# Kernel optimization log

Measured on AMD Instinct MI355X. Metric: run time of the kernel, lower is better.

Reference implementation:

```python
import jax, jax.numpy as jnp
import numpy as np

B, C, T, H, W = 2, 256, 16, 32, 32
NH = 8
GROUPS = 32
EPS = 1e-6


def setup_inputs() -> dict:
    key = jax.random.key(0)
    ks = jax.random.split(key, 10)
    r = lambda k, shape: jax.random.normal(k, shape, dtype=jnp.float32) * 0.02
    return dict(
        x=jax.random.normal(ks[0], (B, C, T, H, W), dtype=jnp.float32),
        gn_gamma=jnp.ones((C,), jnp.float32),
        gn_beta=jnp.zeros((C,), jnp.float32),
        wq_s=r(ks[1], (C, C)), bq_s=jnp.zeros((C,), jnp.float32),
        wk_s=r(ks[2], (C, C)), bk_s=jnp.zeros((C,), jnp.float32),
        wv_s=r(ks[3], (C, C)), bv_s=jnp.zeros((C,), jnp.float32),
        wo_s=r(ks[4], (C, C)), bo_s=jnp.zeros((C,), jnp.float32),
        wq_t=r(ks[5], (C, C)),
        wk_t=r(ks[6], (C, C)),
        wv_t=r(ks[7], (C, C)),
        wf_t=r(ks[8], (C, C)), bf_t=jnp.zeros((C,), jnp.float32),
    )


def group_norm(x, gamma, beta):
    # x: (N, C, H, W), GroupNorm(32, eps=1e-6, affine)
    n, c, h, w = x.shape
    xg = x.reshape(n, GROUPS, c // GROUPS, h, w)
    mu = xg.mean(axis=(2, 3, 4), keepdims=True)
    var = xg.var(axis=(2, 3, 4), keepdims=True)
    xg = (xg - mu) * jax.lax.rsqrt(var + EPS)
    return xg.reshape(n, c, h, w) * gamma[None, :, None, None] + beta[None, :, None, None]


def spatial_attention(x, gn_gamma, gn_beta, wq, bq, wk, bk, wv, bv, wo, bo):
    # ldm SpatialSelfAttention: norm -> 1x1 conv q/k/v -> full HW self-attn -> 1x1 proj -> residual
    n, c, h, w = x.shape
    hf = group_norm(x, gn_gamma, gn_beta).reshape(n, c, h * w)  # (N, C, HW)
    q = jnp.einsum('oc,bcn->bno', wq, hf) + bq                  # (N, HW, C)
    k = jnp.einsum('oc,bcn->bon', wk, hf) + bk[None, :, None]   # (N, C, HW)
    v = jnp.einsum('oc,bcn->bon', wv, hf) + bv[None, :, None]   # (N, C, HW)
    attn = jax.nn.softmax(jnp.einsum('bic,bcj->bij', q, k) * (c ** -0.5), axis=-1)  # (N, HW, HW)
    out = jnp.einsum('bcj,bij->bci', v, attn)                   # (N, C, HW)
    out = jnp.einsum('oc,bcn->bon', wo, out) + bo[None, :, None]
    return x + out.reshape(n, c, h, w)


def axial_temporal_attention(x, wq, wk, wv, wf, bf):
    # x: (B, T, H, W, C); VideoGPT MultiHeadAttention with AxialAttention over T (axial_dim=-4)
    b, t, h, w, c = x.shape
    dk = c // NH

    def heads(y):  # (B,T,H,W,C) -> (B,H,W,NH,T,dk)
        return jnp.transpose(y.reshape(b, t, h, w, NH, dk), (0, 2, 3, 4, 1, 5))

    q = heads(x @ wq)
    k = heads(x @ wk)
    v = heads(x @ wv)
    scores = jnp.einsum('bhwntd,bhwnsd->bhwnts', q, k) / jnp.sqrt(jnp.float32(dk))
    attn = jax.nn.softmax(scores, axis=-1)
    out = jnp.einsum('bhwnts,bhwnsd->bhwntd', attn, v)          # (B,H,W,NH,T,dk)
    out = jnp.transpose(out, (0, 4, 1, 2, 3, 5)).reshape(b, t, h, w, c)
    return out @ wf + bf


def reference(x, gn_gamma, gn_beta, wq_s, bq_s, wk_s, bk_s, wv_s, bv_s, wo_s, bo_s,
              wq_t, wk_t, wv_t, wf_t, bf_t):
    b, c, t, h, w = x.shape
    # spatial branch: torch does a raw reshape (B,C,T,H,W)->(B*T,C,H,W); replicate exactly
    s = spatial_attention(x.reshape(b * t, c, h, w), gn_gamma, gn_beta,
                          wq_s, bq_s, wk_s, bk_s, wv_s, bv_s, wo_s, bo_s)
    s = s.reshape(b, c, t, h, w)
    # temporal branch: channels-last, axial attention over T
    xt = jnp.moveaxis(x, 1, -1)                                 # (B,T,H,W,C)
    tt = axial_temporal_attention(xt, wq_t, wk_t, wv_t, wf_t, bf_t)
    return s + jnp.moveaxis(tt, -1, 1)
```

## Files before the change

### kernel.cpp

```cpp
#include <hip/hip_runtime.h>
#include <stdint.h>

typedef uint16_t u16;
typedef __attribute__((ext_vector_type(8))) short s8v;
typedef __attribute__((ext_vector_type(4))) float f32x4;
typedef __attribute__((ext_vector_type(16))) float f32x16;
typedef __attribute__((ext_vector_type(4))) unsigned short us4;
typedef __attribute__((ext_vector_type(4))) unsigned int u32x4;

__device__ __forceinline__ float bf2f(u16 u) {
  union { uint32_t i; float f; } x; x.i = ((uint32_t)u) << 16; return x.f;
}
__device__ __forceinline__ u16 f2bf(float f) {
  union { float f; uint32_t i; } x; x.f = f;
  uint32_t r = (x.i + 0x7FFFu + ((x.i >> 16) & 1u)) >> 16;
  return (u16)r;
}
__device__ __forceinline__ uint32_t cvtpk(float a, float b) {
  uint32_t r;
  asm("v_cvt_pk_bf16_f32 %0, %1, %2" : "=v"(r) : "v"(a), "v"(b));
  return r;
}
__device__ __forceinline__ void gl2lds16(const u16* g, u16* l) {
  __builtin_amdgcn_global_load_lds(
      (const __attribute__((address_space(1))) uint32_t*)g,
      (__attribute__((address_space(3))) uint32_t*)l, 16, 0, 0);
}

__global__ __launch_bounds__(256) void gn_stats_kernel(const float* __restrict__ x,
                                                       float2* __restrict__ stats) {
  const int tid = threadIdx.x;
  const float* p = x + (long)blockIdx.x * 8192;
  float s = 0.f, s2 = 0.f;
#pragma unroll
  for (int it = 0; it < 8; ++it) {
    float4 v = *(const float4*)(p + it * 1024 + tid * 4);
    s  += v.x + v.y + v.z + v.w;
    s2 += v.x * v.x + v.y * v.y + v.z * v.z + v.w * v.w;
  }
#pragma unroll
  for (int off = 32; off >= 1; off >>= 1) {
    s  += __shfl_down(s, off);
    s2 += __shfl_down(s2, off);
  }
  __shared__ float ps[4], ps2[4];
  const int wv = tid >> 6, lane = tid & 63;
  if (lane == 0) { ps[wv] = s; ps2[wv] = s2; }
  __syncthreads();
  if (tid == 0) {
    float S1 = ps[0] + ps[1] + ps[2] + ps[3];
    float S2 = ps2[0] + ps2[1] + ps2[2] + ps2[3];
    float mean = S1 * (1.f / 8192.f);
    float var = S2 * (1.f / 8192.f) - mean * mean;
    stats[blockIdx.x] = make_float2(mean, rsqrtf(var + 1e-6f));
  }
}

__global__ __launch_bounds__(256) void wprep_kernel(
    const float* __restrict__ s0, const float* __restrict__ s1,
    const float* __restrict__ s2, const float* __restrict__ s3,
    const float* __restrict__ s4, const float* __restrict__ s5,
    const float* __restrict__ s6, const float* __restrict__ s7,
    u16* __restrict__ wbf) {
  const int mat = blockIdx.x, rb = blockIdx.y;
  const float* src = mat==0?s0:mat==1?s1:mat==2?s2:mat==3?s3:mat==4?s4:mat==5?s5:mat==6?s6:s7;
  u16* dst = wbf + mat * 65536 + rb * 16384;
  const int tid = threadIdx.x;
  if (mat < 4) {
    const float* sb = src + rb * 16384;
#pragma unroll
    for (int it = 0; it < 16; ++it) {
      int idx = it * 256 + tid;
      float4 v = *(const float4*)(sb + idx * 4);
      us4 o; o[0]=f2bf(v.x); o[1]=f2bf(v.y); o[2]=f2bf(v.z); o[3]=f2bf(v.w);
      *(us4*)(dst + idx * 4) = o;
    }
  } else {
    __shared__ u16 tl[64][264];
#pragma unroll
    for (int it = 0; it < 16; ++it) {
      int idx = it * 256 + tid;
      int c = idx >> 4, o4 = idx & 15;
      float4 v = *(const float4*)(src + c * 256 + rb * 64 + o4 * 4);
      tl[o4*4+0][c] = f2bf(v.x);
      tl[o4*4+1][c] = f2bf(v.y);
      tl[o4*4+2][c] = f2bf(v.z);
      tl[o4*4+3][c] = f2bf(v.w);
    }
    __syncthreads();
#pragma unroll
    for (int it = 0; it < 16; ++it) {
      int idx = it * 256 + tid;
      int o = idx >> 6, c4 = idx & 63;
      us4 u;
#pragma unroll
      for (int j = 0; j < 4; ++j) u[j] = tl[o][c4*4+j];
      *(us4*)(dst + o * 256 + c4 * 4) = u;
    }
  }
}

__global__ __launch_bounds__(512) void qkv_s_kernel(
    const float* __restrict__ x, const float2* __restrict__ stats,
    const float* __restrict__ gamma, const float* __restrict__ beta,
    const u16* __restrict__ wbf,
    const float* __restrict__ bq, const float* __restrict__ bk, const float* __restrict__ bv,
    u16* __restrict__ qb, u16* __restrict__ kb, u16* __restrict__ vb) {
  __shared__ float gas[256], bes[256];
  __shared__ u16 ALDS[128 * 256];
  __shared__ u16 WLDS[2][64 * 256];
  const int bid = blockIdx.x;
  const int n = bid >> 3, pt = bid & 7;
  const int p0 = pt * 128;
  const int tid = threadIdx.x, w = tid >> 6, lane = tid & 63;
  const int lhi = lane >> 4, llo = lane & 15;
  const long nbase = (long)n * 262144;

  if (tid < 256) {
    float2 st = stats[n * 32 + (tid >> 3)];
    float ga = gamma[tid] * st.y;
    gas[tid] = ga;
    bes[tid] = beta[tid] - st.x * ga;
  }
  __syncthreads();

  const float* xb = x + nbase + p0;
#pragma unroll
  for (int it = 0; it < 16; ++it) {
    int idx = it * 512 + tid;
    int p = idx & 127, c4 = idx >> 7;
    us4 o;
#pragma unroll
    for (int j = 0; j < 4; ++j) {
      int c = c4 * 4 + j;
      float v = xb[(long)c * 1024 + p];
      o[j] = f2bf(v * gas[c] + bes[c]);
    }
    int ch = c4 >> 1;
    *(us4*)&ALDS[p * 256 + ((ch ^ (p & 7)) << 3) + ((c4 & 1) << 2)] = o;
  }
  __syncthreads();

  const int arow = w * 16 + llo;
  s8v qa[8];
#pragma unroll
  for (int kk = 0; kk < 8; ++kk)
    qa[kk] = *(const s8v*)&ALDS[arow * 256 + (((kk * 4 + lhi) ^ (arow & 7)) << 3)];

  auto stageW = [&](int t, int bu) {
    const u16* wsrc = wbf + (t >> 2) * 65536 + (long)(t & 3) * 16384;
#pragma unroll
    for (int ii = 0; ii < 4; ++ii) {
      int i0 = (w * 4 + ii) * 64;
      int g = i0 + lane;
      int row = g >> 5, ch = g & 31;
      gl2lds16(wsrc + row * 256 + ((ch ^ (row & 7)) << 3), &WLDS[bu][i0 * 8]);
    }
  };

  stageW(0, 0);
  __syncthreads();

  u16* vtl = ALDS;
  for (int t = 0; t < 12; ++t) {
    const int cur = t & 1;
    if (t < 11) stageW(t + 1, cur ^ 1);
    f32x4 acc[4] = {};
#pragma unroll
    for (int kk = 0; kk < 8; ++kk)
#pragma unroll
      for (int nf = 0; nf < 4; ++nf) {
        int row = nf * 16 + llo;
        s8v bfr = *(const s8v*)&WLDS[cur][row * 256 + (((kk * 4 + lhi) ^ (row & 7)) << 3)];
        acc[nf] = __builtin_amdgcn_mfma_f32_16x16x32_bf16(qa[kk], bfr, acc[nf], 0, 0, 0);
      }
    const int o0 = (t & 3) * 64;
    if (t < 8) {
      u16* dstb = (t < 4) ? qb : kb;
      const float* bias = (t < 4) ? bq : bk;
#pragma unroll
      for (int nf = 0; nf < 4; ++nf) {
        int o = o0 + nf * 16 + llo;
        float b_ = bias[o];
#pragma unroll
        for (int r = 0; r < 4; ++r)
          dstb[nbase + (long)(p0 + w * 16 + lhi * 4 + r) * 256 + o] = f2bf(acc[nf][r] + b_);
      }
    } else {
#pragma unroll
      for (int nf = 0; nf < 4; ++nf) {
        int o = nf * 16 + llo;
        float b_ = bv[o0 + o];
#pragma unroll
        for (int r = 0; r < 4; ++r)
          vtl[o * 136 + w * 16 + lhi * 4 + r] = f2bf(acc[nf][r] + b_);
      }
      __syncthreads();
#pragma unroll
      for (int ii = 0; ii < 4; ++ii) {
        int i = ii * 512 + tid;
        int o = i >> 5, p4 = (i & 31) * 4;
        us4 u;
#pragma unroll
        for (int j = 0; j < 4; ++j) u[j] = vtl[o * 136 + p4 + j];
        *(us4*)(vb + nbase + (long)(o0 + o) * 1024 + p0 + p4) = u;
      }
    }
    __syncthreads();
  }
}

__global__ __launch_bounds__(256, 1) void flash_kernel(const u16* __restrict__ qb,
                                                       const u16* __restrict__ kb,
                                                       const u16* __restrict__ vb,
                                                       u16* __restrict__ attb) {
  const int wg = blockIdx.x;
  const int swz = (wg & 7) * 32 + (wg >> 3);
  const int n = swz >> 3, qt = swz & 7;
  const int tid = threadIdx.x, w = tid >> 6, lane = tid & 63;
  const int q5 = lane & 31, h = lane >> 5;
  const long nbase = (long)n * 262144;

  __shared__ u16 Kb[2][64 * 256];
  __shared__ u16 Vb[2][256 * 64];

  const int qrow = qt * 128 + w * 32 + q5;
  const u16* qr = qb + nbase + (long)qrow * 256 + h * 8;
  s8v qa[16];
#pragma unroll
  for (int kk = 0; kk < 16; ++kk) qa[kk] = *(const s8v*)(qr + kk * 16);

  f32x16 oaccT[8] = {};
  float m_ = -3.4e38f, l_ = 0.f;
  constexpr float CEXP = 0.09016844f;

  auto stageKV = [&](int jt2, int b) {
    const u16* kbase = kb + nbase + (long)jt2 * 64 * 256;
    const u16* vbase = vb + nbase + (long)jt2 * 64;
#pragma unroll
    for (int ii = 0; ii < 8; ++ii) {
      int slot = ii * 256 + tid;
      int row = slot >> 5, ch = slot & 31;
      gl2lds16(kbase + (long)row * 256 + ((ch ^ (row & 7)) << 3), &Kb[b][slot * 8]);
    }
#pragma unroll
    for (int ii = 0; ii < 8; ++ii) {
      int slot = ii * 256 + tid;
      int c = slot >> 3, ch = slot & 7;
      gl2lds16(vbase + (long)c * 1024 + ((ch ^ (c & 7)) << 3), &Vb[b][slot * 8]);
    }
  };

  stageKV(0, 0);
  __syncthreads();

  for (int jt = 0; jt < 16; ++jt) {
    const int cur = jt & 1;
    if (jt < 15) stageKV(jt + 1, cur ^ 1);

    f32x16 sacc[2] = {};
#pragma unroll
    for (int kk = 0; kk < 16; ++kk) {
#pragma unroll
      for (int f = 0; f < 2; ++f) {
        int krow = f * 32 + q5;
        s8v kfr = *(const s8v*)&Kb[cur][krow * 256 + (((kk * 2 + h) ^ (q5 & 7)) << 3)];
        sacc[f] = __builtin_amdgcn_mfma_f32_32x32x16_bf16(kfr, qa[kk], sacc[f], 0, 0, 0);
      }
    }
    float pm = sacc[0][0];
#pragma unroll
    for (int f = 0; f < 2; ++f)
#pragma unroll
      for (int r = 0; r < 16; ++r) pm = fmaxf(pm, sacc[f][r]);
    pm = fmaxf(pm, __shfl_xor(pm, 32));
    if (!__all(pm <= m_ + 128.f)) {
      float scf = exp2f((m_ - pm) * CEXP);
      l_ *= scf;
#pragma unroll
      for (int cf = 0; cf < 8; ++cf)
#pragma unroll
        for (int r = 0; r < 16; ++r) oaccT[cf][r] *= scf;
      m_ = pm;
    }
    float rs = 0.f;
#pragma unroll
    for (int f = 0; f < 2; ++f)
#pragma unroll
      for (int r = 0; r < 16; ++r) {
        float p = exp2f((sacc[f][r] - m_) * CEXP);
        sacc[f][r] = p;
        rs += p;
      }
    rs += __shfl_xor(rs, 32);
    l_ += rs;
    uint32_t pk[2][4][2];
#pragma unroll
    for (int f = 0; f < 2; ++f)
#pragma unroll
      for (int g = 0; g < 4; ++g) {
        pk[f][g][0] = cvtpk(sacc[f][4 * g + 0], sacc[f][4 * g + 1]);
        pk[f][g][1] = cvtpk(sacc[f][4 * g + 2], sacc[f][4 * g + 3]);
      }
#pragma unroll
    for (int js = 0; js < 4; ++js) {
      const int f = js >> 1, g0 = 2 * (js & 1);
      uint32_t own0 = h ? pk[f][g0 + 1][0] : pk[f][g0][0];
      uint32_t own1 = h ? pk[f][g0 + 1][1] : pk[f][g0][1];
      uint32_t snd0 = h ? pk[f][g0][0] : pk[f][g0 + 1][0];
      uint32_t snd1 = h ? pk[f][g0][1] : pk[f][g0 + 1][1];
      uint32_t rcv0 = __shfl_xor(snd0, 32);
      uint32_t rcv1 = __shfl_xor(snd1, 32);
      u32x4 pw;
      pw[0] = h ? rcv0 : own0;
      pw[1] = h ? rcv1 : own1;
      pw[2] = h ? own0 : rcv0;
      pw[3] = h ? own1 : rcv1;
      s8v pa = __builtin_bit_cast(s8v, pw);
#pragma unroll
      for (int cf = 0; cf < 8; ++cf) {
        int c = cf * 32 + q5;
        s8v vfr = *(const s8v*)&Vb[cur][c * 64 + (((js * 2 + h) ^ (q5 & 7)) << 3)];
        oaccT[cf] = __builtin_amdgcn_mfma_f32_32x32x16_bf16(vfr, pa, oaccT[cf], 0, 0, 0);
      }
    }
    __syncthreads();
  }
  float inv = 1.f / l_;
  u16* tl = &Kb[0][0];
  __syncthreads();
  const int myq = w * 32 + q5;
#pragma unroll
  for (int cf = 0; cf < 8; ++cf)
#pragma unroll
    for (int g = 0; g < 4; ++g) {
      uint32_t w0 = cvtpk(oaccT[cf][4 * g + 0] * inv, oaccT[cf][4 * g + 1] * inv);
      uint32_t w1 = cvtpk(oaccT[cf][4 * g + 2] * inv, oaccT[cf][4 * g + 3] * inv);
      int ch = (cf * 4 + g) ^ (myq & 7);
      uint2 val; val.x = w0; val.y = w1;
      *(uint2*)&tl[myq * 256 + ch * 8 + h * 4] = val;
    }
  __syncthreads();
  const int qo = tid >> 1, hr = tid & 1;
  u16* obase = attb + nbase + (long)(qt * 128 + qo) * 256;
#pragma unroll
  for (int u = 0; u < 16; ++u) {
    int c16 = hr * 16 + u;
    u32x4 v = *(const u32x4*)&tl[qo * 256 + ((c16 ^ (qo & 7)) << 3)];
    *(u32x4*)(obase + c16 * 8) = v;
  }
}

__global__ __launch_bounds__(512) void qkv_t_kernel(
    const float* __restrict__ x, const u16* __restrict__ wbf,
    u16* __restrict__ qt, u16* __restrict__ kt, u16* __restrict__ vt) {
  __shared__ u16 ALDS[128 * 256];
  __shared__ u16 WLDS[2][64 * 256];
  const int bid = blockIdx.x;
  const int b = bid >> 7, st = bid & 127;
  const int s0 = st * 128;
  const int tid = threadIdx.x, w = tid >> 6, lane = tid & 63;
  const int lhi = lane >> 4, llo = lane & 15;
  const long bbase = (long)b * 4194304;

  const float* xb = x + bbase + s0;
#pragma unroll
  for (int it = 0; it < 16; ++it) {
    int idx = it * 512 + tid;
    int p = idx & 127, c4 = idx >> 7;
    us4 o;
#pragma unroll
    for (int j = 0; j < 4; ++j)
      o[j] = f2bf(xb[(long)(c4 * 4 + j) * 16384 + p]);
    int ch = c4 >> 1;
    *(us4*)&ALDS[p * 256 + ((ch ^ (p & 7)) << 3) + ((c4 & 1) << 2)] = o;
  }
  __syncthreads();
  const int arow = w * 16 + llo;
  s8v qa[8];
#pragma unroll
  for (int kk = 0; kk < 8; ++kk)
    qa[kk] = *(const s8v*)&ALDS[arow * 256 + (((kk * 4 + lhi) ^ (arow & 7)) << 3)];

  auto stageW = [&](int t, int bu) {
    const u16* wsrc = wbf + (4 + (t >> 2)) * 65536 + (long)(t & 3) * 16384;
#pragma unroll
    for (int ii = 0; ii < 4; ++ii) {
      int i0 = (w * 4 + ii) * 64;
      int g = i0 + lane;
      int row = g >> 5, ch = g & 31;
      gl2lds16(wsrc + row * 256 + ((ch ^ (row & 7)) << 3), &WLDS[bu][i0 * 8]);
    }
  };
  stageW(0, 0);
  __syncthreads();
  for (int t = 0; t < 12; ++t) {
    const int cur = t & 1;
    if (t < 11) stageW(t + 1, cur ^ 1);
    f32x4 acc[4] = {};
#pragma unroll
    for (int kk = 0; kk < 8; ++kk)
#pragma unroll
      for (int nf = 0; nf < 4; ++nf) {
        int row = nf * 16 + llo;
        s8v bb = *(const s8v*)&WLDS[cur][row * 256 + (((kk * 4 + lhi) ^ (row & 7)) << 3)];
        acc[nf] = __builtin_amdgcn_mfma_f32_16x16x32_bf16(qa[kk], bb, acc[nf], 0, 0, 0);
      }
    u16* dstb = (t < 4) ? qt : (t < 8) ? kt : vt;
    const int o0 = (t & 3) * 64;
#pragma unroll
    for (int nf = 0; nf < 4; ++nf) {
      int o = o0 + nf * 16 + llo;
#pragma unroll
      for (int r = 0; r < 4; ++r)
        dstb[bbase + (long)(s0 + w * 16 + lhi * 4 + r) * 256 + o] = f2bf(acc[nf][r]);
    }
    __syncthreads();
  }
}

__global__ __launch_bounds__(256) void tattn_kernel(const u16* __restrict__ qt,
                                                    const u16* __restrict__ kt,
                                                    const u16* __restrict__ vt,
                                                    u16* __restrict__ ot) {
  const int bi = blockIdx.x >> 10, hw = blockIdx.x & 1023;
  const long base = (long)bi * 4194304 + (long)hw * 256;
  __shared__ float qs[16][260], ks[16][260], vs[16][260];
  __shared__ u16 os[16][256];
  const int tid = threadIdx.x;
#pragma unroll
  for (int it = 0; it < 4; ++it) {
    int idx = it * 256 + tid;
    int t = idx >> 6, cv = idx & 63;
    long g = base + (long)t * 262144 + cv * 4;
    us4 a = *(const us4*)(qt + g);
    us4 b = *(const us4*)(kt + g);
    us4 c = *(const us4*)(vt + g);
#pragma unroll
    for (int j = 0; j < 4; ++j) {
      qs[t][cv * 4 + j] = bf2f(a[j]);
      ks[t][cv * 4 + j] = bf2f(b[j]);
      vs[t][cv * 4 + j] = bf2f(c[j]);
    }
  }
  __syncthreads();
  if (tid < 128) {
    const int h = tid >> 4, t = tid & 15;
    const int c0 = h * 32;
    float sc[16];
    float mx = -3.4e38f;
#pragma unroll
    for (int t2 = 0; t2 < 16; ++t2) {
      float d = 0.f;
#pragma unroll
      for (int dd = 0; dd < 32; ++dd) d += qs[t][c0 + dd] * ks[t2][c0 + dd];
      sc[t2] = d * 0.17677669529663687f;
      mx = fmaxf(mx, sc[t2]);
    }
    float sum = 0.f;
#pragma unroll
    for (int t2 = 0; t2 < 16; ++t2) { sc[t2] = __expf(sc[t2] - mx); sum += sc[t2]; }
    float inv = 1.f / sum;
#pragma unroll
    for (int dd = 0; dd < 32; ++dd) {
      float o = 0.f;
#pragma unroll
      for (int t2 = 0; t2 < 16; ++t2) o += sc[t2] * vs[t2][c0 + dd];
      os[t][c0 + dd] = f2bf(o * inv);
    }
  }
  __syncthreads();
#pragma unroll
  for (int it = 0; it < 4; ++it) {
    int idx = it * 256 + tid;
    int t = idx >> 6, cv = idx & 63;
    us4 o4;
#pragma unroll
    for (int j = 0; j < 4; ++j) o4[j] = os[t][cv * 4 + j];
    *(us4*)(ot + base + (long)t * 262144 + cv * 4) = o4;
  }
}

__global__ __launch_bounds__(512) void tfinal_kernel(
    const u16* __restrict__ ott, const u16* __restrict__ wbf,
    u16* __restrict__ tmpT) {
  __shared__ u16 ALDS[128 * 256];
  __shared__ u16 WLDS[2][64 * 256];
  const int bid = blockIdx.x;
  const int b = bid >> 7, st = bid & 127;
  const int s0 = st * 128;
  const int tid = threadIdx.x, w = tid >> 6, lane = tid & 63;
  const int lhi = lane >> 4, llo = lane & 15;
  const long bbase = (long)b * 4194304;

  const u16* otS = ott + bbase + (long)s0 * 256;
#pragma unroll
  for (int ii = 0; ii < 8; ++ii) {
    int i0 = (w * 8 + ii) * 64;
    int g = i0 + lane;
    int row = g >> 5, ch = g & 31;
    gl2lds16(otS + row * 256 + ((ch ^ (row & 7)) << 3), &ALDS[i0 * 8]);
  }
  __syncthreads();
  const int arow = w * 16 + llo;
  s8v qa[8];
#pragma unroll
  for (int kk = 0; kk < 8; ++kk)
    qa[kk] = *(const s8v*)&ALDS[arow * 256 + (((kk * 4 + lhi) ^ (arow & 7)) << 3)];

  auto stageW = [&](int t, int bu) {
    const u16* wsrc = wbf + 7 * 65536 + (long)t * 16384;
#pragma unroll
    for (int ii = 0; ii < 4; ++ii) {
      int i0 = (w * 4 + ii) * 64;
      int g = i0 + lane;
      int row = g >> 5, ch = g & 31;
      gl2lds16(wsrc + row * 256 + ((ch ^ (row & 7)) << 3), &WLDS[bu][i0 * 8]);
    }
  };
  stageW(0, 0);
  __syncthreads();
  u16* vtl = ALDS;
  for (int t = 0; t < 4; ++t) {
    const int cur = t & 1;
    if (t < 3) stageW(t + 1, cur ^ 1);
    f32x4 acc[4] = {};
#pragma unroll
    for (int kk = 0; kk < 8; ++kk)
#pragma unroll
      for (int nf = 0; nf < 4; ++nf) {
        int row = nf * 16 + llo;
        s8v bb = *(const s8v*)&WLDS[cur][row * 256 + (((kk * 4 + lhi) ^ (row & 7)) << 3)];
        acc[nf] = __builtin_amdgcn_mfma_f32_16x16x32_bf16(qa[kk], bb, acc[nf], 0, 0, 0);
      }
#pragma unroll
    for (int nf = 0; nf < 4; ++nf) {
      int o = nf * 16 + llo;
#pragma unroll
      for (int r = 0; r < 4; ++r)
        vtl[o * 136 + w * 16 + lhi * 4 + r] = f2bf(acc[nf][r]);
    }
    __syncthreads();
    const int o0 = t * 64;
#pragma unroll
    for (int ii = 0; ii < 4; ++ii) {
      int i = ii * 512 + tid;
      int o = i >> 5, p4 = (i & 31) * 4;
      us4 uu;
#pragma unroll
      for (int j = 0; j < 4; ++j) uu[j] = vtl[o * 136 + p4 + j];
      *(us4*)(tmpT + bbase + (long)(o0 + o) * 16384 + s0 + p4) = uu;
    }
    __syncthreads();
  }
}

__global__ __launch_bounds__(256) void outproj_kernel(
    const float* __restrict__ x, const u16* __restrict__ attb,
    const u16* __restrict__ tmpT, const u16* __restrict__ wbf,
    const float* __restrict__ bo, const float* __restrict__ bf,
    float* __restrict__ out) {
  __shared__ u16 attL[64 * 256];
  const int u = blockIdx.x;
  const int wkx = (u & 7) * 256 + (u >> 3);
  const int otile = wkx & 3, pt = (wkx >> 2) & 15, n = wkx >> 6;
  const int b = n >> 4;
  const int o0 = otile * 64, p0 = pt * 64;
  const int tid = threadIdx.x, w = tid >> 6, lane = tid & 63;
  const int lhi = lane >> 4, llo = lane & 15;
  const long nbase = (long)n * 262144;

  const u16* attS = attb + nbase + (long)p0 * 256;
#pragma unroll
  for (int ii = 0; ii < 8; ++ii) {
    int i0 = (w * 8 + ii) * 64;
    int g = i0 + lane;
    int row = g >> 5, ch = g & 31;
    gl2lds16(attS + row * 256 + ((ch ^ (row & 7)) << 3), &attL[i0 * 8]);
  }
  const u16* woR = wbf + 3 * 65536 + (long)(o0 + w * 16 + llo) * 256;
  s8v woa[8];
#pragma unroll
  for (int kk = 0; kk < 8; ++kk)
    woa[kk] = *(const s8v*)(woR + kk * 32 + lhi * 8);
  __syncthreads();
  f32x4 acc[4] = {};
#pragma unroll
  for (int kk = 0; kk < 8; ++kk)
#pragma unroll
    for (int nf = 0; nf < 4; ++nf) {
      int row = nf * 16 + llo;
      s8v b1 = *(const s8v*)&attL[row * 256 + (((kk * 4 + lhi) ^ (row & 7)) << 3)];
      acc[nf] = __builtin_amdgcn_mfma_f32_16x16x32_bf16(woa[kk], b1, acc[nf], 0, 0, 0);
    }
#pragma unroll
  for (int r = 0; r < 4; ++r) {
    int cp = o0 + w * 16 + lhi * 4 + r;
    int co = ((n & 15) << 4) + (cp >> 4);
    int tt = cp & 15;
    float bias = bo[cp] + bf[co];
    const u16* tr = tmpT + (long)b * 4194304 + (long)co * 16384 + tt * 1024 + p0;
    const float* xr = x + nbase + (long)cp * 1024 + p0;
    float* orow = out + nbase + (long)cp * 1024 + p0;
#pragma unroll
    for (int nf = 0; nf < 4; ++nf) {
      int p = nf * 16 + llo;
      orow[p] = acc[nf][r] + bias + xr[p] + bf2f(tr[p]);
    }
  }
}

extern "C" void kernel_launch(void* const* d_in, const int* in_sizes, int n_in,
                              void* d_out, int out_size, void* d_ws, size_t ws_size,
                              hipStream_t stream) {
  const float* x     = (const float*)d_in[0];
  const float* gam   = (const float*)d_in[1];
  const float* bet   = (const float*)d_in[2];
  const float* wq_s  = (const float*)d_in[3];
  const float* bq_s  = (const float*)d_in[4];
  const float* wk_s  = (const float*)d_in[5];
  const float* bk_s  = (const float*)d_in[6];
  const float* wv_s  = (const float*)d_in[7];
  const float* bv_s  = (const float*)d_in[8];
  const float* wo_s  = (const float*)d_in[9];
  const float* bo_s  = (const float*)d_in[10];
  const float* wq_t  = (const float*)d_in[11];
  const float* wk_t  = (const float*)d_in[12];
  const float* wv_t  = (const float*)d_in[13];
  const float* wf_t  = (const float*)d_in[14];
  const float* bf_t  = (const float*)d_in[15];
  float* out = (float*)d_out;

  u16* qb   = (u16*)d_ws;
  u16* kb   = qb + 8388608;
  u16* vb   = kb + 8388608;
  u16* attb = vb + 8388608;
  u16* ottb = attb + 8388608;
  u16* wbf  = ottb + 8388608;
  float2* stats = (float2*)(wbf + 524288);
  u16* qt = qb; u16* kt = kb; u16* vt = vb;
  u16* tmpT = qb;

  gn_stats_kernel<<<1024, 256, 0, stream>>>(x, stats);
  wprep_kernel<<<dim3(8, 4), 256, 0, stream>>>(wq_s, wk_s, wv_s, wo_s,
                                               wq_t, wk_t, wv_t, wf_t, wbf);
  qkv_s_kernel<<<256, 512, 0, stream>>>(x, stats, gam, bet, wbf,
                                        bq_s, bk_s, bv_s, qb, kb, vb);
  flash_kernel<<<256, 256, 0, stream>>>(qb, kb, vb, attb);
  qkv_t_kernel<<<256, 512, 0, stream>>>(x, wbf, qt, kt, vt);
  tattn_kernel<<<2048, 256, 0, stream>>>(qt, kt, vt, ottb);
  tfinal_kernel<<<256, 512, 0, stream>>>(ottb, wbf, tmpT);
  outproj_kernel<<<2048, 256, 0, stream>>>(x, attb, tmpT, wbf, bo_s, bf_t, out);
}
```

Baseline: 203.0 us.

## Split flash attention KV tiles across two wave groups with LDS merge

The flash kernel goes from 256 to 512 threads. Two groups of four waves each take half of every 64-key tile for the same 128 queries, and their partial softmax states and outputs are merged through LDS at the end. s_setprio hints are also added around the MFMA loops. The aim is to double the waves per CU, hiding latency and keeping more MFMA work in flight. The cost is extra LDS traffic, a final merge step, and a lower register budget per thread under the new launch bounds.

```diff
diff --git a/kernel.cpp b/kernel.cpp
--- a/kernel.cpp
+++ b/kernel.cpp
@@ -210,7 +210,7 @@
   }
 }
 
-__global__ __launch_bounds__(256, 1) void flash_kernel(const u16* __restrict__ qb,
+__global__ __launch_bounds__(512, 2) void flash_kernel(const u16* __restrict__ qb,
                                                        const u16* __restrict__ kb,
                                                        const u16* __restrict__ vb,
                                                        u16* __restrict__ attb) {
@@ -219,12 +219,15 @@
   const int n = swz >> 3, qt = swz & 7;
   const int tid = threadIdx.x, w = tid >> 6, lane = tid & 63;
   const int q5 = lane & 31, h = lane >> 5;
+  const int wq = w & 3;
+  const int kh = w >> 2;
   const long nbase = (long)n * 262144;
 
-  __shared__ u16 Kb[2][64 * 256];
-  __shared__ u16 Vb[2][256 * 64];
-
-  const int qrow = qt * 128 + w * 32 + q5;
+  __shared__ u16 Kb[2][16384];
+  __shared__ u16 Vb[2][16384];
+  __shared__ float2 mlbuf[128];
+
+  const int qrow = qt * 128 + wq * 32 + q5;
   const u16* qr = qb + nbase + (long)qrow * 256 + h * 8;
   s8v qa[16];
 #pragma unroll
@@ -235,44 +238,41 @@
   constexpr float CEXP = 0.09016844f;
 
   auto stageKV = [&](int jt2, int b) {
-    const u16* kbase = kb + nbase + (long)jt2 * 64 * 256;
+    const u16* kbase = kb + nbase + (long)jt2 * 16384;
     const u16* vbase = vb + nbase + (long)jt2 * 64;
 #pragma unroll
-    for (int ii = 0; ii < 8; ++ii) {
-      int slot = ii * 256 + tid;
-      int row = slot >> 5, ch = slot & 31;
-      gl2lds16(kbase + (long)row * 256 + ((ch ^ (row & 7)) << 3), &Kb[b][slot * 8]);
-    }
-#pragma unroll
-    for (int ii = 0; ii < 8; ++ii) {
-      int slot = ii * 256 + tid;
-      int c = slot >> 3, ch = slot & 7;
-      gl2lds16(vbase + (long)c * 1024 + ((ch ^ (c & 7)) << 3), &Vb[b][slot * 8]);
+    for (int ii = 0; ii < 4; ++ii) {
+      int s = ii * 512 + tid;
+      int row = s >> 5, ch = s & 31;
+      gl2lds16(kbase + (long)row * 256 + ((ch ^ (row & 7)) << 3), &Kb[b][s * 8]);
+    }
+#pragma unroll
+    for (int ii = 0; ii < 4; ++ii) {
+      int s = ii * 512 + tid;
+      int c = s >> 3, ch = s & 7;
+      gl2lds16(vbase + (long)c * 1024 + ((ch ^ (c & 7)) << 3), &Vb[b][s * 8]);
     }
   };
 
   stageKV(0, 0);
   __syncthreads();
 
+  const int krow = kh * 32 + q5;
   for (int jt = 0; jt < 16; ++jt) {
     const int cur = jt & 1;
     if (jt < 15) stageKV(jt + 1, cur ^ 1);
 
-    f32x16 sacc[2] = {};
+    f32x16 sacc = {};
+    __builtin_amdgcn_s_setprio(1);
 #pragma unroll
     for (int kk = 0; kk < 16; ++kk) {
-#pragma unroll
-      for (int f = 0; f < 2; ++f) {
-        int krow = f * 32 + q5;
-        s8v kfr = *(const s8v*)&Kb[cur][krow * 256 + (((kk * 2 + h) ^ (q5 & 7)) << 3)];
-        sacc[f] = __builtin_amdgcn_mfma_f32_32x32x16_bf16(kfr, qa[kk], sacc[f], 0, 0, 0);
-      }
-    }
-    float pm = sacc[0][0];
-#pragma unroll
-    for (int f = 0; f < 2; ++f)
-#pragma unroll
-      for (int r = 0; r < 16; ++r) pm = fmaxf(pm, sacc[f][r]);
+      s8v kfr = *(const s8v*)&Kb[cur][krow * 256 + (((kk * 2 + h) ^ (krow & 7)) << 3)];
+      sacc = __builtin_amdgcn_mfma_f32_32x32x16_bf16(kfr, qa[kk], sacc, 0, 0, 0);
+    }
+    __builtin_amdgcn_s_setprio(0);
+    float pm = sacc[0];
+#pragma unroll
+    for (int r = 1; r < 16; ++r) pm = fmaxf(pm, sacc[r]);
     pm = fmaxf(pm, __shfl_xor(pm, 32));
     if (!__all(pm <= m_ + 128.f)) {
       float scf = exp2f((m_ - pm) * CEXP);
@@ -285,30 +285,25 @@
     }
     float rs = 0.f;
 #pragma unroll
-    for (int f = 0; f < 2; ++f)
-#pragma unroll
-      for (int r = 0; r < 16; ++r) {
-        float p = exp2f((sacc[f][r] - m_) * CEXP);
-        sacc[f][r] = p;
-        rs += p;
-      }
+    for (int r = 0; r < 16; ++r) {
+      float p = exp2f((sacc[r] - m_) * CEXP);
+      sacc[r] = p;
+      rs += p;
+    }
     rs += __shfl_xor(rs, 32);
     l_ += rs;
-    uint32_t pk[2][4][2];
-#pragma unroll
-    for (int f = 0; f < 2; ++f)
-#pragma unroll
-      for (int g = 0; g < 4; ++g) {
-        pk[f][g][0] = cvtpk(sacc[f][4 * g + 0], sacc[f][4 * g + 1]);
-        pk[f][g][1] = cvtpk(sacc[f][4 * g + 2], sacc[f][4 * g + 3]);
-      }
-#pragma unroll
-    for (int js = 0; js < 4; ++js) {
-      const int f = js >> 1, g0 = 2 * (js & 1);
-      uint32_t own0 = h ? pk[f][g0 + 1][0] : pk[f][g0][0];
-      uint32_t own1 = h ? pk[f][g0 + 1][1] : pk[f][g0][1];
-      uint32_t snd0 = h ? pk[f][g0][0] : pk[f][g0 + 1][0];
-      uint32_t snd1 = h ? pk[f][g0][1] : pk[f][g0 + 1][1];
+    uint32_t pk[4][2];
+#pragma unroll
+    for (int g = 0; g < 4; ++g) {
+      pk[g][0] = cvtpk(sacc[4 * g + 0], sacc[4 * g + 1]);
+      pk[g][1] = cvtpk(sacc[4 * g + 2], sacc[4 * g + 3]);
+    }
+#pragma unroll
+    for (int js = 0; js < 2; ++js) {
+      uint32_t own0 = pk[2 * js + h][0];
+      uint32_t own1 = pk[2 * js + h][1];
+      uint32_t snd0 = pk[2 * js + (h ^ 1)][0];
+      uint32_t snd1 = pk[2 * js + (h ^ 1)][1];
       uint32_t rcv0 = __shfl_xor(snd0, 32);
       uint32_t rcv1 = __shfl_xor(snd1, 32);
       u32x4 pw;
@@ -317,37 +312,64 @@
       pw[2] = h ? own0 : rcv0;
       pw[3] = h ? own1 : rcv1;
       s8v pa = __builtin_bit_cast(s8v, pw);
+      __builtin_amdgcn_s_setprio(1);
 #pragma unroll
       for (int cf = 0; cf < 8; ++cf) {
         int c = cf * 32 + q5;
-        s8v vfr = *(const s8v*)&Vb[cur][c * 64 + (((js * 2 + h) ^ (q5 & 7)) << 3)];
+        s8v vfr = *(const s8v*)&Vb[cur][c * 64 + (((kh * 4 + js * 2 + h) ^ (c & 7)) << 3)];
         oaccT[cf] = __builtin_amdgcn_mfma_f32_32x32x16_bf16(vfr, pa, oaccT[cf], 0, 0, 0);
       }
+      __builtin_amdgcn_s_setprio(0);
     }
     __syncthreads();
   }
-  float inv = 1.f / l_;
+  uint32_t* OH = (uint32_t*)&Vb[0][0];
   u16* tl = &Kb[0][0];
-  __syncthreads();
-  const int myq = w * 32 + q5;
-#pragma unroll
-  for (int cf = 0; cf < 8; ++cf)
-#pragma unroll
-    for (int g = 0; g < 4; ++g) {
-      uint32_t w0 = cvtpk(oaccT[cf][4 * g + 0] * inv, oaccT[cf][4 * g + 1] * inv);
-      uint32_t w1 = cvtpk(oaccT[cf][4 * g + 2] * inv, oaccT[cf][4 * g + 3] * inv);
-      int ch = (cf * 4 + g) ^ (myq & 7);
-      uint2 val; val.x = w0; val.y = w1;
-      *(uint2*)&tl[myq * 256 + ch * 8 + h * 4] = val;
-    }
-  __syncthreads();
-  const int qo = tid >> 1, hr = tid & 1;
+  if (kh == 1) {
+#pragma unroll
+    for (int cf = 0; cf < 8; ++cf)
+#pragma unroll
+      for (int i = 0; i < 8; ++i)
+        OH[(((wq * 8 + cf) * 8 + i) * 2 + h) * 32 + q5] =
+            cvtpk(oaccT[cf][2 * i], oaccT[cf][2 * i + 1]);
+    if (h == 0) mlbuf[wq * 32 + q5] = make_float2(m_, l_);
+  }
+  __syncthreads();
+  if (kh == 0) {
+    float2 pml = mlbuf[wq * 32 + q5];
+    float M = fmaxf(m_, pml.x);
+    float alo = exp2f((m_ - M) * CEXP);
+    float ahi = exp2f((pml.x - M) * CEXP);
+    float linv = 1.f / (l_ * alo + pml.y * ahi);
+    float slo = alo * linv, shi = ahi * linv;
+    const int myq = wq * 32 + q5;
+#pragma unroll
+    for (int cf = 0; cf < 8; ++cf) {
+      float v[16];
+#pragma unroll
+      for (int i = 0; i < 8; ++i) {
+        uint32_t pv = OH[(((wq * 8 + cf) * 8 + i) * 2 + h) * 32 + q5];
+        v[2 * i]     = oaccT[cf][2 * i] * slo + bf2f((u16)(pv & 0xffff)) * shi;
+        v[2 * i + 1] = oaccT[cf][2 * i + 1] * slo + bf2f((u16)(pv >> 16)) * shi;
+      }
+#pragma unroll
+      for (int g = 0; g < 4; ++g) {
+        uint2 val;
+        val.x = cvtpk(v[4 * g + 0], v[4 * g + 1]);
+        val.y = cvtpk(v[4 * g + 2], v[4 * g + 3]);
+        int ch = (cf * 4 + g) ^ (myq & 7);
+        *(uint2*)&tl[myq * 256 + ch * 8 + h * 4] = val;
+      }
+    }
+  }
+  __syncthreads();
+  const int qo = tid >> 2, qu = tid & 3;
   u16* obase = attb + nbase + (long)(qt * 128 + qo) * 256;
 #pragma unroll
-  for (int u = 0; u < 16; ++u) {
-    int c16 = hr * 16 + u;
-    u32x4 v = *(const u32x4*)&tl[qo * 256 + ((c16 ^ (qo & 7)) << 3)];
-    *(u32x4*)(obase + c16 * 8) = v;
+  for (int u = 0; u < 8; ++u) {
+    int c16 = qu * 8 + u;
+    u32x4 vv = *(const u32x4*)&tl[qo * 256 + ((c16 ^ (qo & 7)) << 3)];
+    *(u32x4*)(obase + c16 * 8) = vv;
   }
 }
 
@@ -646,7 +668,7 @@
                                                wq_t, wk_t, wv_t, wf_t, wbf);
   qkv_s_kernel<<<256, 512, 0, stream>>>(x, stats, gam, bet, wbf,
                                         bq_s, bk_s, bv_s, qb, kb, vb);
-  flash_kernel<<<256, 256, 0, stream>>>(qb, kb, vb, attb);
+  flash_kernel<<<256, 512, 0, stream>>>(qb, kb, vb, attb);
   qkv_t_kernel<<<256, 512, 0, stream>>>(x, wbf, qt, kt, vt);
   tattn_kernel<<<2048, 256, 0, stream>>>(qt, kt, vt, ottb);
   tfinal_kernel<<<256, 512, 0, stream>>>(ottb, wbf, tmpT);
```

Result: slower. 218.1 us (+7.4%).
